# Optimization experiments

Hardware: AMD Instinct MI355X
Metric: run time of the kernel (lower is better)

## Reference

```python
import jax, jax.numpy as jnp
import numpy as np

VOXEL_SIZE = 0.05  # init kwarg


def setup_inputs() -> dict:
    key = jax.random.key(0)
    N, B = 4_194_304, 16
    # coords uniform in [0, 5)^3 -> ~100^3 voxel cells per scene at voxel_size=0.05
    coord = jax.random.uniform(key, (N, 3), dtype=jnp.float32) * 5.0
    # cumulative batch offsets (equal-sized scenes), as pointops expects
    offset = (jnp.arange(1, B + 1, dtype=jnp.int32) * (N // B)).astype(jnp.int32)
    return {"coord": coord, "offset": offset}


def _voxel_mean(coord, offset, voxel_size):
    """Faithful jax port of voxelize_helper + segment_csr(mean) + batch2offset.

    Returns:
      n_p    [N,3]  voxel-mean coords, padded with zeros beyond n_voxels
      n_o    [B]    cumulative voxel counts per batch (batch2offset)
      counts [N]    points per voxel (idx_ptr = concat([0], cumsum(counts[valid])))
    """
    N = coord.shape[0]
    B = offset.shape[0]
    # batch id per point from cumulative offsets
    batch = jnp.searchsorted(offset, jnp.arange(N), side='right')  # [N]
    # start = per-batch min coord (start=None path of voxelize_helper)
    start = jax.ops.segment_min(coord, batch, num_segments=B)      # [B,3]
    grid = jnp.floor((coord - start[batch]) / voxel_size).astype(jnp.int32)  # [N,3]
    G = jnp.max(grid) + 1  # grid extent (per-axis upper bound)
    # linearized cluster key: unique per (batch, gx, gy, gz)
    ckey = ((batch * G + grid[:, 0]) * G + grid[:, 1]) * G + grid[:, 2]
    fill = B * G * G * G  # sentinel beyond any real key
    # sorted unique cluster keys == CSR segment order after sorting cluster indices
    uniq, inv = jnp.unique(ckey, return_inverse=True, size=N, fill_value=fill)
    # fused gather + segment-mean (equivalent to coord[sorted_idx] -> segment_csr mean)
    seg_sum = jax.ops.segment_sum(coord, inv, num_segments=N)                 # [N,3]
    counts = jax.ops.segment_sum(jnp.ones((N,), coord.dtype), inv, num_segments=N)
    n_p = seg_sum / jnp.maximum(counts, 1.0)[:, None]
    # batch id per voxel -> batch2offset (cumulative voxel counts)
    valid = uniq < fill
    vbatch = jnp.where(valid, uniq // (G * G * G), B)
    per_batch = jax.ops.segment_sum(valid.astype(jnp.int32), vbatch, num_segments=B + 1)[:B]
    n_o = jnp.cumsum(per_batch)
    return n_p, n_o, counts.astype(jnp.int32)


def reference(coord, offset):
    return _voxel_mean(coord, offset, VOXEL_SIZE)
```

## Files before the change

kernel.cpp:

```cpp
#include <hip/hip_runtime.h>
#include <stdint.h>


typedef unsigned int uint;
typedef unsigned long long u64;

#define VS 0.05f
#define QSCALE (4096.0f / VS)
#define QINV  (VS / 4096.0f)
#define NBUCKET 2048
#define NBLK_P 256
#define DENSE_MAX 8192

__device__ __forceinline__ uint f2m(float f) {
    uint b = __float_as_uint(f);
    return (b & 0x80000000u) ? ~b : (b | 0x80000000u);
}
__device__ __forceinline__ float m2f(uint m) {
    uint b = (m & 0x80000000u) ? (m & 0x7fffffffu) : ~m;
    return __uint_as_float(b);
}

__global__ void k_init(uint* start_m, int B3) {
    int i = blockIdx.x * blockDim.x + threadIdx.x;
    if (i < B3) start_m[i] = 0xFFFFFFFFu;
}

__global__ void __launch_bounds__(256)
k_minmax(const float* __restrict__ coord, const int* __restrict__ offset,
         int N, int B, uint* start_m) {
    __shared__ uint smin[768];
    __shared__ int soff[256];
    int t = threadIdx.x;
    int nb3 = B * 3;
    for (int j = t; j < B; j += 256) soff[j] = offset[j];
    for (int j = t; j < nb3; j += 256) smin[j] = 0xFFFFFFFFu;
    __syncthreads();

    int F = 3 * N;
    int NQ = F >> 2;
    int per = (NQ + gridDim.x - 1) / gridDim.x;
    int qlo = blockIdx.x * per;
    int qhi = min(NQ, qlo + per);
    const float4* __restrict__ c4 = reinterpret_cast<const float4*>(coord);

    bool fast = false;
    int bU = 0;
    if (qlo < qhi) {
        int pF = (4 * qlo) / 3;
        int pL = (4 * qhi - 1) / 3;
        int bF = 0, bL = 0;
        for (int j = 0; j < B; ++j) {
            bF += (pF >= soff[j]) ? 1 : 0;
            bL += (pL >= soff[j]) ? 1 : 0;
        }
        fast = (bF == bL);
        bU = bF;
    }

    if (fast) {
        int q = qlo + t;
        int p0 = q % 3;
        float s0 = INFINITY, s1 = INFINITY, s2 = INFINITY;
        for (;;) {
            if (q >= qhi) break;
            float4 v = c4[q];
            s0 = fminf(s0, fminf(v.x, v.w)); s1 = fminf(s1, v.y); s2 = fminf(s2, v.z);
            q += 256;
            if (q >= qhi) break;
            v = c4[q];
            s1 = fminf(s1, fminf(v.x, v.w)); s2 = fminf(s2, v.y); s0 = fminf(s0, v.z);
            q += 256;
            if (q >= qhi) break;
            v = c4[q];
            s2 = fminf(s2, fminf(v.x, v.w)); s0 = fminf(s0, v.y); s1 = fminf(s1, v.z);
            q += 256;
        }
        float ax, ay, az;
        if (p0 == 0)      { ax = s0; ay = s1; az = s2; }
        else if (p0 == 1) { ax = s2; ay = s0; az = s1; }
        else              { ax = s1; ay = s2; az = s0; }
        for (int d = 32; d; d >>= 1) {
            ax = fminf(ax, __shfl_xor(ax, d));
            ay = fminf(ay, __shfl_xor(ay, d));
            az = fminf(az, __shfl_xor(az, d));
        }
        if ((t & 63) == 0 && ax < INFINITY) {
            atomicMin(&smin[bU * 3 + 0], f2m(ax));
            atomicMin(&smin[bU * 3 + 1], f2m(ay));
            atomicMin(&smin[bU * 3 + 2], f2m(az));
        }
    } else {
        for (int q = qlo + t; q < qhi; q += 256) {
            float4 v = c4[q];
            int e = 4 * q;
            float vals[4] = {v.x, v.y, v.z, v.w};
#pragma unroll
            for (int k = 0; k < 4; ++k) {
                int ee = e + k;
                int pt = ee / 3;
                int axis = ee - 3 * pt;
                int b = 0;
                for (int j = 0; j < B; ++j) b += (pt >= soff[j]) ? 1 : 0;
                atomicMin(&smin[b * 3 + axis], f2m(vals[k]));
            }
        }
    }

    if (blockIdx.x == 0) {
        for (int ee = 4 * NQ + t; ee < F; ee += 256) {
            int pt = ee / 3;
            int axis = ee - 3 * pt;
            int b = 0;
            for (int j = 0; j < B; ++j) b += (pt >= soff[j]) ? 1 : 0;
            atomicMin(&smin[b * 3 + axis], f2m(coord[ee]));
        }
    }
    __syncthreads();
    for (int j = t; j < nb3; j += 256) {
        uint mn = smin[j];
        if (mn != 0xFFFFFFFFu) atomicMin(&start_m[j], mn);
    }
}


__global__ void __launch_bounds__(1024)
k_count(const float* __restrict__ coord, const int* __restrict__ offset,
        int N, int B, const uint* __restrict__ start_m, uint* __restrict__ histm) {
    __shared__ uint hist[NBUCKET];
    __shared__ int soff[16];
    __shared__ float sstart[48];
    int t = threadIdx.x;
    if (t < B) soff[t] = offset[t];
    if (t < B * 3) sstart[t] = m2f(start_m[t]);
    for (int j = t; j < NBUCKET; j += 1024) hist[j] = 0;
    __syncthreads();
    int chunk = (N + gridDim.x - 1) / gridDim.x;
    int lo = blockIdx.x * chunk, hi = min(N, lo + chunk);
    int bLo = 0, bHi = 0;
    for (int j = 0; j < B; ++j) {
        bLo += (lo >= soff[j]) ? 1 : 0;
        bHi += (hi - 1 >= soff[j]) ? 1 : 0;
    }
    if (lo < hi && bLo == bHi && (lo & 3) == 0) {
        int b = bLo;
        float sx = sstart[b * 3];
        int base = b << 7;
        const float4* __restrict__ c4 = reinterpret_cast<const float4*>(coord);
        int gEnd = hi >> 2;
        for (int g = (lo >> 2) + t; g < gEnd; g += 1024) {
            float4 v0 = c4[3 * g], v1 = c4[3 * g + 1], v2 = c4[3 * g + 2];
            int gx0 = min((int)floorf((v0.x - sx) / VS), 127);
            int gx1 = min((int)floorf((v0.w - sx) / VS), 127);
            int gx2 = min((int)floorf((v1.z - sx) / VS), 127);
            int gx3 = min((int)floorf((v2.y - sx) / VS), 127);
            atomicAdd(&hist[base | gx0], 1u);
            atomicAdd(&hist[base | gx1], 1u);
            atomicAdd(&hist[base | gx2], 1u);
            atomicAdd(&hist[base | gx3], 1u);
        }
        for (int i = (gEnd << 2) + t; i < hi; i += 1024) {
            float x = coord[3 * i];
            int gx = min((int)floorf((x - sx) / VS), 127);
            atomicAdd(&hist[base | gx], 1u);
        }
    } else {
        for (int i = lo + t; i < hi; i += 1024) {
            float x = coord[3 * i];
            int b = 0;
            for (int j = 0; j < B; ++j) b += (i >= soff[j]) ? 1 : 0;
            int gx = min((int)floorf((x - sstart[b * 3]) / VS), 127);
            atomicAdd(&hist[(b << 7) | gx], 1u);
        }
    }
    __syncthreads();
    for (int j = t; j < NBUCKET; j += 1024)
        histm[(size_t)j * NBLK_P + blockIdx.x] = hist[j];
}

__global__ void k_scanrow(uint* __restrict__ histm, uint* __restrict__ tot) {
    __shared__ uint sc[256];
    uint* row = histm + (size_t)blockIdx.x * NBLK_P;
    int t = threadIdx.x;
    uint v = row[t];
    sc[t] = v;
    __syncthreads();
    for (int d = 1; d < 256; d <<= 1) {
        uint add = (t >= d) ? sc[t - d] : 0;
        __syncthreads();
        sc[t] += add;
        __syncthreads();
    }
    row[t] = sc[t] - v;
    if (t == 255) tot[blockIdx.x] = sc[255];
}

__global__ void k_scan2048(const uint* __restrict__ in, uint* __restrict__ out) {
    __shared__ uint p[1024];
    int t = threadIdx.x;
    uint a = in[2 * t], bb = in[2 * t + 1];
    p[t] = a + bb;
    __syncthreads();
    for (int d = 1; d < 1024; d <<= 1) {
        uint add = (t >= d) ? p[t - d] : 0;
        __syncthreads();
        p[t] += add;
        __syncthreads();
    }
    uint ex = p[t] - (a + bb);
    out[2 * t] = ex;
    out[2 * t + 1] = ex + a;
    if (t == 1023) out[2048] = p[1023];
}

__global__ void k_scan2048b(const uint* __restrict__ in, uint* __restrict__ out,
                            int B, float* __restrict__ no_out) {
    __shared__ uint p[1024];
    int t = threadIdx.x;
    uint a = in[2 * t], bb = in[2 * t + 1];
    p[t] = a + bb;
    __syncthreads();
    for (int d = 1; d < 1024; d <<= 1) {
        uint add = (t >= d) ? p[t - d] : 0;
        __syncthreads();
        p[t] += add;
        __syncthreads();
    }
    uint ex = p[t] - (a + bb);
    out[2 * t] = ex;
    out[2 * t + 1] = ex + a;
    if (t == 1023) out[2048] = p[1023];
    if (t < B) no_out[t] = (float)p[((t + 1) << 6) - 1];
}

__device__ __forceinline__ void part_point(float x, float y, float z, int b,
                                           float sx, float sy, float sz,
                                           uint* cursor, u64* __restrict__ recs) {
    int gx = min((int)floorf((x - sx) / VS), 127);
    int gy = min((int)floorf((y - sy) / VS), 127);
    int gz = min((int)floorf((z - sz) / VS), 127);
    float fx = fmaxf(x - (sx + (float)gx * VS), 0.0f);
    float fy = fmaxf(y - (sy + (float)gy * VS), 0.0f);
    float fz = fmaxf(z - (sz + (float)gz * VS), 0.0f);
    uint ux = min((uint)(fx * QSCALE + 0.5f), 4095u);
    uint uy = min((uint)(fy * QSCALE + 0.5f), 4095u);
    uint uz = min((uint)(fz * QSCALE + 0.5f), 4095u);
    uint cell = ((uint)gy << 7) | (uint)gz;
    u64 rec = ((u64)cell << 36) | ((u64)ux << 24) | ((u64)uy << 12) | (u64)uz;
    uint q = ((uint)b << 7) | (uint)gx;
    uint slot = atomicAdd(&cursor[q], 1u);
    recs[slot] = rec;
}

__global__ void __launch_bounds__(1024)
k_partition(const float* __restrict__ coord, const int* __restrict__ offset,
            int N, int B, const uint* __restrict__ start_m,
            const uint* __restrict__ histm, const uint* __restrict__ bucket_base,
            u64* __restrict__ recs) {
    __shared__ uint cursor[NBUCKET];
    __shared__ int soff[16];
    __shared__ float sstart[48];
    int t = threadIdx.x;
    if (t < B) soff[t] = offset[t];
    if (t < B * 3) sstart[t] = m2f(start_m[t]);
    for (int j = t; j < NBUCKET; j += 1024)
        cursor[j] = bucket_base[j] + histm[(size_t)j * NBLK_P + blockIdx.x];
    __syncthreads();
    int chunk = (N + gridDim.x - 1) / gridDim.x;
    int lo = blockIdx.x * chunk, hi = min(N, lo + chunk);
    int bLo = 0, bHi = 0;
    for (int j = 0; j < B; ++j) {
        bLo += (lo >= soff[j]) ? 1 : 0;
        bHi += (hi - 1 >= soff[j]) ? 1 : 0;
    }
    if (lo < hi && bLo == bHi && (lo & 3) == 0) {
        int b = bLo;
        float sx = sstart[b * 3 + 0], sy = sstart[b * 3 + 1], sz = sstart[b * 3 + 2];
        const float4* __restrict__ c4 = reinterpret_cast<const float4*>(coord);
        int gEnd = hi >> 2;
        for (int g = (lo >> 2) + t; g < gEnd; g += 1024) {
            float4 v0 = c4[3 * g], v1 = c4[3 * g + 1], v2 = c4[3 * g + 2];
            part_point(v0.x, v0.y, v0.z, b, sx, sy, sz, cursor, recs);
            part_point(v0.w, v1.x, v1.y, b, sx, sy, sz, cursor, recs);
            part_point(v1.z, v1.w, v2.x, b, sx, sy, sz, cursor, recs);
            part_point(v2.y, v2.z, v2.w, b, sx, sy, sz, cursor, recs);
        }
        for (int i = (gEnd << 2) + t; i < hi; i += 1024) {
            float x = coord[3 * i + 0], y = coord[3 * i + 1], z = coord[3 * i + 2];
            part_point(x, y, z, b, sx, sy, sz, cursor, recs);
        }
    } else {
        for (int i = lo + t; i < hi; i += 1024) {
            float x = coord[3 * i + 0], y = coord[3 * i + 1], z = coord[3 * i + 2];
            int b = 0;
            for (int j = 0; j < B; ++j) b += (i >= soff[j]) ? 1 : 0;
            part_point(x, y, z, b, sstart[b * 3 + 0], sstart[b * 3 + 1],
                       sstart[b * 3 + 2], cursor, recs);
        }
    }
}

__global__ void k_vox(const u64* __restrict__ recs, const uint* __restrict__ bucket_base,
                      uint* __restrict__ voxcount, uint* __restrict__ gmask) {
    __shared__ uint bits[512];
    __shared__ uint wsum[4];
    int q = blockIdx.x;
    uint lo = bucket_base[q], hi = bucket_base[q + 1];
    for (int j = threadIdx.x; j < 512; j += blockDim.x) bits[j] = 0;
    __syncthreads();
    for (uint i = lo + threadIdx.x; i < hi; i += blockDim.x) {
        uint c = (uint)(recs[i] >> 36);
        atomicOr(&bits[c >> 5], 1u << (c & 31));
    }
    __syncthreads();
    uint s = 0;
    for (int w = threadIdx.x; w < 512; w += blockDim.x) {
        uint m = bits[w];
        gmask[(size_t)q * 512 + w] = m;
        s += __popc(m);
    }
    for (int d = 32; d; d >>= 1) s += __shfl_xor(s, d);
    if ((threadIdx.x & 63) == 0) wsum[threadIdx.x >> 6] = s;
    __syncthreads();
    if (threadIdx.x == 0) voxcount[q] = wsum[0] + wsum[1] + wsum[2] + wsum[3];
}

__global__ void __launch_bounds__(1024)
k_emit2(const u64* __restrict__ recs, const uint* __restrict__ bucket_base,
        const uint* __restrict__ voxscan, const uint* __restrict__ gmask,
        const uint* __restrict__ start_m, int N, int B, int out_total,
        float* __restrict__ np_out, float* __restrict__ cnt_out,
        float* __restrict__ out) {
    int t = threadIdx.x;
    if (blockIdx.x >= NBUCKET) {
        uint total = voxscan[NBUCKET];
        int zb = blockIdx.x - NBUCKET;
        int stride = (gridDim.x - NBUCKET) * 1024;
        int tid = zb * 1024 + t;
        for (int j = 3 * (int)total + tid; j < 3 * N; j += stride) np_out[j] = 0.0f;
        for (int j = (int)total + tid; j < N; j += stride) cnt_out[j] = 0.0f;
        for (int j = 4 * N + B + tid; j < out_total; j += stride) out[j] = 0.0f;
        return;
    }
    __shared__ u64 dense[DENSE_MAX];
    __shared__ uint mask[512], wrank[512];
    __shared__ uint wtot[8], woff[9];
    __shared__ float sstart[48];
    int q = blockIdx.x;
    uint lo = bucket_base[q], hi = bucket_base[q + 1];
    if (lo == hi) return;
    if (t < 48) sstart[t] = m2f(start_m[t]);
    uint m = 0, c = 0;
    if (t < 512) {
        m = gmask[(size_t)q * 512 + t];
        mask[t] = m;
        c = __popc(m);
    }
    uint sc = c;
    for (int d = 1; d < 64; d <<= 1) {
        uint nb = __shfl_up(sc, d, 64);
        if ((t & 63) >= d) sc += nb;
    }
    if (t < 512 && (t & 63) == 63) wtot[t >> 6] = sc;
    __syncthreads();
    if (t == 0) {
        uint r = 0;
        for (int k = 0; k < 8; ++k) { woff[k] = r; r += wtot[k]; }
        woff[8] = r;
    }
    __syncthreads();
    if (t < 512) wrank[t] = sc - c + woff[t >> 6];
    uint vc = woff[8];
    uint base_r = voxscan[q];
    int b = q >> 7, gx = q & 127;
    float cx = sstart[b * 3 + 0] + (float)gx * VS;
    float sy = sstart[b * 3 + 1], sz = sstart[b * 3 + 2];
    for (uint segbase = 0; segbase < vc; segbase += DENSE_MAX) {
        uint seglen = min(vc - segbase, (uint)DENSE_MAX);
        for (uint j = t; j < seglen; j += 1024) dense[j] = 0ull;
        __syncthreads();
        for (uint i = lo + t; i < hi; i += 1024) {
            u64 rec = recs[i];
            uint cc = (uint)(rec >> 36);
            uint w = cc >> 5, bit = cc & 31;
            uint r = wrank[w] + __popc(mask[w] & ((1u << bit) - 1u));
            if (r >= segbase && r < segbase + seglen) {
                u64 enc = (((rec >> 24) & 0xFFFull) << 46) | (((rec >> 12) & 0xFFFull) << 28)
                        | ((rec & 0xFFFull) << 10) | 1ull;
                atomicAdd(&dense[r - segbase], enc);
            }
        }
        __syncthreads();
        for (uint rr = segbase + t; rr < segbase + seglen; rr += 1024) {
            uint l2 = 0, h2 = 511;
            while (l2 < h2) {
                uint mid = (l2 + h2 + 1) >> 1;
                if (wrank[mid] <= rr) l2 = mid; else h2 = mid - 1;
            }
            uint w = l2;
            uint idx = rr - wrank[w];
            uint mm = mask[w], bit = 0, cp;
            cp = __popc(mm & 0xFFFFu); if (idx >= cp) { idx -= cp; bit += 16; mm >>= 16; }
            cp = __popc(mm & 0xFFu);   if (idx >= cp) { idx -= cp; bit += 8;  mm >>= 8; }
            cp = __popc(mm & 0xFu);    if (idx >= cp) { idx -= cp; bit += 4;  mm >>= 4; }
            cp = __popc(mm & 0x3u);    if (idx >= cp) { idx -= cp; bit += 2;  mm >>= 2; }
            cp = __popc(mm & 0x1u);    if (idx >= cp) { bit += 1; }
            uint cell = (w << 5) + bit;
            uint gy = cell >> 7, gz = cell & 127u;
            u64 p = dense[rr - segbase];
            float cnt = (float)(uint)(p & 1023ull);
            float inv = 1.0f / fmaxf(cnt, 1.0f);
            uint uz = (uint)((p >> 10) & 0x3FFFFull);
            uint uy = (uint)((p >> 28) & 0x3FFFFull);
            uint ux = (uint)(p >> 46);
            uint r_out = base_r + rr;
            np_out[3 * r_out + 0] = cx + ((float)ux * QINV) * inv;
            np_out[3 * r_out + 1] = sy + (float)gy * VS + ((float)uy * QINV) * inv;
            np_out[3 * r_out + 2] = sz + (float)gz * VS + ((float)uz * QINV) * inv;
            cnt_out[r_out] = cnt;
        }
        __syncthreads();
    }
}


__device__ __forceinline__ void point_grid(const float* __restrict__ coord, int i,
                                           const int* soff, const float* sstart, int B,
                                           float& x, float& y, float& z,
                                           int& b, int& gx, int& gy, int& gz) {
    x = coord[3 * i + 0]; y = coord[3 * i + 1]; z = coord[3 * i + 2];
    b = 0;
    for (int j = 0; j < B; ++j) b += (i >= soff[j]) ? 1 : 0;
    gx = min((int)floorf((x - sstart[b * 3 + 0]) / VS), 127);
    gy = min((int)floorf((y - sstart[b * 3 + 1]) / VS), 127);
    gz = min((int)floorf((z - sstart[b * 3 + 2]) / VS), 127);
}

__device__ __forceinline__ u64 frac12(float x, float y, float z,
                                      const float* sstart, int b,
                                      int gx, int gy, int gz) {
    float fx = fmaxf(x - (sstart[b * 3 + 0] + (float)gx * VS), 0.0f);
    float fy = fmaxf(y - (sstart[b * 3 + 1] + (float)gy * VS), 0.0f);
    float fz = fmaxf(z - (sstart[b * 3 + 2] + (float)gz * VS), 0.0f);
    uint ux = min((uint)(fx * QSCALE + 0.5f), 4095u);
    uint uy = min((uint)(fy * QSCALE + 0.5f), 4095u);
    uint uz = min((uint)(fz * QSCALE + 0.5f), 4095u);
    return ((u64)ux << 24) | ((u64)uy << 12) | (u64)uz;
}

__global__ void k_hist(const float* __restrict__ coord, const int* __restrict__ offset,
                       int N, int B, const uint* __restrict__ start_m,
                       uint* __restrict__ mask) {
    __shared__ int soff[256];
    __shared__ float sstart[768];
    for (int j = threadIdx.x; j < B; j += blockDim.x) soff[j] = offset[j];
    for (int j = threadIdx.x; j < B * 3; j += blockDim.x) sstart[j] = m2f(start_m[j]);
    __syncthreads();
    int i = blockIdx.x * blockDim.x + threadIdx.x;
    if (i >= N) return;
    float x, y, z; int b, gx, gy, gz;
    point_grid(coord, i, soff, sstart, B, x, y, z, b, gx, gy, gz);
    uint key = ((uint)b << 21) | ((uint)gx << 14) | ((uint)gy << 7) | (uint)gz;
    atomicOr(&mask[key >> 5], 1u << (key & 31));
}

__global__ void k_scan1(const uint* __restrict__ mask, uint* __restrict__ partial) {
    int base = blockIdx.x * 1024 + threadIdx.x * 4;
    uint4 m = *(const uint4*)(mask + base);
    uint s = __popc(m.x) + __popc(m.y) + __popc(m.z) + __popc(m.w);
    for (int d = 32; d; d >>= 1) s += __shfl_xor(s, d);
    __shared__ uint wsum[4];
    if ((threadIdx.x & 63) == 0) wsum[threadIdx.x >> 6] = s;
    __syncthreads();
    if (threadIdx.x == 0) partial[blockIdx.x] = wsum[0] + wsum[1] + wsum[2] + wsum[3];
}

__global__ void k_scan2(uint* partial, int P, uint* total) {
    __shared__ uint t[256];
    uint carry = 0;
    for (int base = 0; base < P; base += 256) {
        int j = base + threadIdx.x;
        uint v = (j < P) ? partial[j] : 0;
        t[threadIdx.x] = v;
        __syncthreads();
        for (int d = 1; d < 256; d <<= 1) {
            uint add = (threadIdx.x >= d) ? t[threadIdx.x - d] : 0;
            __syncthreads();
            t[threadIdx.x] += add;
            __syncthreads();
        }
        uint inc = t[threadIdx.x];
        uint chunk = t[255];
        if (j < P) partial[j] = carry + inc - v;
        __syncthreads();
        carry += chunk;
    }
    if (threadIdx.x == 0) *total = carry;
}

__global__ void k_scan3(const uint* __restrict__ mask, const uint* __restrict__ partial,
                        uint* __restrict__ wordrank) {
    int base = blockIdx.x * 1024 + threadIdx.x * 4;
    uint4 m = *(const uint4*)(mask + base);
    uint c0 = __popc(m.x), c1 = __popc(m.y), c2 = __popc(m.z), c3 = __popc(m.w);
    uint s = c0 + c1 + c2 + c3;
    __shared__ uint t[256];
    t[threadIdx.x] = s;
    __syncthreads();
    for (int d = 1; d < 256; d <<= 1) {
        uint add = (threadIdx.x >= d) ? t[threadIdx.x - d] : 0;
        __syncthreads();
        t[threadIdx.x] += add;
        __syncthreads();
    }
    uint ex = t[threadIdx.x] - s + partial[blockIdx.x];
    uint4 r;
    r.x = ex; r.y = ex + c0; r.z = ex + c0 + c1; r.w = ex + c0 + c1 + c2;
    *(uint4*)(wordrank + base) = r;
}

__global__ void k_no(const uint* mask, const uint* wordrank, const uint* total,
                     float* no_out, int B, int W) {
    int b = blockIdx.x * blockDim.x + threadIdx.x;
    if (b >= B) return;
    long long idx = (long long)(b + 1) << 21;
    uint w = (uint)(idx >> 5);
    uint v;
    if (w >= (uint)W) v = *total;
    else v = wordrank[w];
    no_out[b] = (float)v;
}

__global__ void k_accum_sparse(const float* __restrict__ coord, const int* __restrict__ offset,
                               int N, int B, const uint* __restrict__ start_m,
                               const uint* __restrict__ mask, const uint* __restrict__ wordrank,
                               u64* __restrict__ packed) {
    __shared__ int soff[256];
    __shared__ float sstart[768];
    for (int j = threadIdx.x; j < B; j += blockDim.x) soff[j] = offset[j];
    for (int j = threadIdx.x; j < B * 3; j += blockDim.x) sstart[j] = m2f(start_m[j]);
    __syncthreads();
    int i = blockIdx.x * blockDim.x + threadIdx.x;
    if (i >= N) return;
    float x, y, z; int b, gx, gy, gz;
    point_grid(coord, i, soff, sstart, B, x, y, z, b, gx, gy, gz);
    uint key = ((uint)b << 21) | ((uint)gx << 14) | ((uint)gy << 7) | (uint)gz;
    uint w = key >> 5, bit = key & 31;
    uint r = wordrank[w] + __popc(mask[w] & ((1u << bit) - 1u));
    u64 f = frac12(x, y, z, sstart, b, gx, gy, gz);
    u64 enc = (((f >> 24) & 0xFFFull) << 46) | (((f >> 12) & 0xFFFull) << 28)
            | ((f & 0xFFFull) << 10) | 1ull;
    atomicAdd(&packed[r], enc);
}

__global__ void k_decode_sparse(const uint* __restrict__ mask, const uint* __restrict__ wordrank,
                                const uint* __restrict__ start_m,
                                const u64* __restrict__ packed, int W,
                                float* __restrict__ np_out, float* __restrict__ cnt_out) {
    __shared__ float sstart[48];
    for (int j = threadIdx.x; j < 48; j += blockDim.x) sstart[j] = m2f(start_m[j]);
    __syncthreads();
    int w = blockIdx.x * blockDim.x + threadIdx.x;
    if (w >= W) return;
    uint m = mask[w];
    if (m == 0) return;
    uint r = wordrank[w];
    uint kbase = (uint)w << 5;
    while (m) {
        uint bit = (uint)__ffs(m) - 1u;
        m &= m - 1u;
        uint key = kbase + bit;
        u64 p = packed[r];
        float cnt = (float)(uint)(p & 1023ull);
        float inv = 1.0f / fmaxf(cnt, 1.0f);
        uint uz = (uint)((p >> 10) & 0x3FFFFull);
        uint uy = (uint)((p >> 28) & 0x3FFFFull);
        uint ux = (uint)(p >> 46);
        uint b = key >> 21;
        uint gx = (key >> 14) & 127u;
        uint gy = (key >> 7) & 127u;
        uint gz = key & 127u;
        np_out[3 * r + 0] = sstart[b * 3 + 0] + (float)gx * VS + ((float)ux * QINV) * inv;
        np_out[3 * r + 1] = sstart[b * 3 + 1] + (float)gy * VS + ((float)uy * QINV) * inv;
        np_out[3 * r + 2] = sstart[b * 3 + 2] + (float)gz * VS + ((float)uz * QINV) * inv;
        cnt_out[r] = cnt;
        ++r;
    }
}

extern "C" void kernel_launch(void* const* d_in, const int* in_sizes, int n_in,
                              void* d_out, int out_size, void* d_ws, size_t ws_size,
                              hipStream_t stream) {
    const float* coord = (const float*)d_in[0];
    const int* offset = (const int*)d_in[1];
    int N = in_sizes[0] / 3;
    int B = in_sizes[1];

    float* out = (float*)d_out;
    float* np_out = out;
    float* no_out = out + (size_t)3 * N;
    float* cnt_out = no_out + B;

    uint8_t* base = (uint8_t*)d_ws;
    uint* start_m = (uint*)base;
    uint* total = start_m + (size_t)B * 3;

    uintptr_t p = (uintptr_t)(total + 1);
    p = (p + 255) & ~(uintptr_t)255;
    uint* histm = (uint*)p;          p += (size_t)NBUCKET * NBLK_P * 4;
    p = (p + 255) & ~(uintptr_t)255;
    uint* tot = (uint*)p;            p += (size_t)NBUCKET * 4;
    p = (p + 255) & ~(uintptr_t)255;
    uint* bucket_base = (uint*)p;    p += (size_t)(NBUCKET + 1) * 4;
    p = (p + 255) & ~(uintptr_t)255;
    uint* voxcount = (uint*)p;       p += (size_t)NBUCKET * 4;
    p = (p + 255) & ~(uintptr_t)255;
    uint* voxscan = (uint*)p;        p += (size_t)(NBUCKET + 1) * 4;
    p = (p + 255) & ~(uintptr_t)255;
    uint* gmask = (uint*)p;          p += (size_t)NBUCKET * 512 * 4;
    p = (p + 255) & ~(uintptr_t)255;
    u64* recs = (u64*)p;             p += (size_t)N * 8;
    size_t need_part = p - (uintptr_t)base;

    k_init<<<(B * 3 + 255) / 256, 256, 0, stream>>>(start_m, B * 3);
    k_minmax<<<2048, 256, 0, stream>>>(coord, offset, N, B, start_m);

    if (B <= 16 && ws_size >= need_part) {
        k_count<<<NBLK_P, 1024, 0, stream>>>(coord, offset, N, B, start_m, histm);
        k_scanrow<<<NBUCKET, 256, 0, stream>>>(histm, tot);
        k_scan2048<<<1, 1024, 0, stream>>>(tot, bucket_base);
        k_partition<<<NBLK_P, 1024, 0, stream>>>(coord, offset, N, B, start_m, histm,
                                                 bucket_base, recs);
        k_vox<<<NBUCKET, 256, 0, stream>>>(recs, bucket_base, voxcount, gmask);
        k_scan2048b<<<1, 1024, 0, stream>>>(voxcount, voxscan, B, no_out);
        k_emit2<<<NBUCKET + 1024, 1024, 0, stream>>>(recs, bucket_base, voxscan, gmask,
                                                     start_m, N, B, out_size,
                                                     np_out, cnt_out, out);
    } else {
        hipMemsetAsync(d_out, 0, (size_t)out_size * sizeof(float), stream);
        size_t W = (size_t)B << 16;
        int nblk1 = (int)(W / 1024);
        uintptr_t sp = (uintptr_t)(total + 1);
        sp = (sp + 255) & ~(uintptr_t)255;
        uint* partial = (uint*)sp;   sp += (size_t)nblk1 * 4;
        sp = (sp + 255) & ~(uintptr_t)255;
        uint* mask = (uint*)sp;      sp += W * 4;
        sp = (sp + 255) & ~(uintptr_t)255;
        uint* wordrank = (uint*)sp;  sp += W * 4;
        sp = (sp + 255) & ~(uintptr_t)255;
        u64* packed = (u64*)sp;
        int nb = (N + 255) / 256;
        hipMemsetAsync(mask, 0, W * sizeof(uint), stream);
        hipMemsetAsync(packed, 0, (size_t)N * sizeof(u64), stream);
        k_hist<<<nb, 256, 0, stream>>>(coord, offset, N, B, start_m, mask);
        k_scan1<<<nblk1, 256, 0, stream>>>(mask, partial);
        k_scan2<<<1, 256, 0, stream>>>(partial, nblk1, total);
        k_scan3<<<nblk1, 256, 0, stream>>>(mask, partial, wordrank);
        k_no<<<(B + 63) / 64, 64, 0, stream>>>(mask, wordrank, total, no_out, B, (int)W);
        k_accum_sparse<<<nb, 256, 0, stream>>>(coord, offset, N, B, start_m, mask,
                                               wordrank, packed);
        k_decode_sparse<<<(int)((W + 255) / 256), 256, 0, stream>>>(mask, wordrank, start_m,
                                                                    packed, (int)W,
                                                                    np_out, cnt_out);
    }
}
```

Measured before the change: 199.3 us.

## Compute packed records once in count pass and scatter them from temp buffer

The count kernel now computes the full packed voxel record per point, including the bucket id in the top bits, and writes it to a temporary array while building the histogram. A new scatter kernel reads these records and places them with shared-memory cursors, so the coordinates are no longer re-read and the cell math is not recomputed in the partition pass. The cost is an extra N*8-byte write and read of the temp buffer plus more workspace; the consumers now mask the cell field because of the added bucket bits.

```diff
diff --git a/kernel.cpp b/kernel.cpp
--- a/kernel.cpp
+++ b/kernel.cpp
@@ -124,118 +124,9 @@
 }
 
 
-__global__ void __launch_bounds__(1024)
-k_count(const float* __restrict__ coord, const int* __restrict__ offset,
-        int N, int B, const uint* __restrict__ start_m, uint* __restrict__ histm) {
-    __shared__ uint hist[NBUCKET];
-    __shared__ int soff[16];
-    __shared__ float sstart[48];
-    int t = threadIdx.x;
-    if (t < B) soff[t] = offset[t];
-    if (t < B * 3) sstart[t] = m2f(start_m[t]);
-    for (int j = t; j < NBUCKET; j += 1024) hist[j] = 0;
-    __syncthreads();
-    int chunk = (N + gridDim.x - 1) / gridDim.x;
-    int lo = blockIdx.x * chunk, hi = min(N, lo + chunk);
-    int bLo = 0, bHi = 0;
-    for (int j = 0; j < B; ++j) {
-        bLo += (lo >= soff[j]) ? 1 : 0;
-        bHi += (hi - 1 >= soff[j]) ? 1 : 0;
-    }
-    if (lo < hi && bLo == bHi && (lo & 3) == 0) {
-        int b = bLo;
-        float sx = sstart[b * 3];
-        int base = b << 7;
-        const float4* __restrict__ c4 = reinterpret_cast<const float4*>(coord);
-        int gEnd = hi >> 2;
-        for (int g = (lo >> 2) + t; g < gEnd; g += 1024) {
-            float4 v0 = c4[3 * g], v1 = c4[3 * g + 1], v2 = c4[3 * g + 2];
-            int gx0 = min((int)floorf((v0.x - sx) / VS), 127);
-            int gx1 = min((int)floorf((v0.w - sx) / VS), 127);
-            int gx2 = min((int)floorf((v1.z - sx) / VS), 127);
-            int gx3 = min((int)floorf((v2.y - sx) / VS), 127);
-            atomicAdd(&hist[base | gx0], 1u);
-            atomicAdd(&hist[base | gx1], 1u);
-            atomicAdd(&hist[base | gx2], 1u);
-            atomicAdd(&hist[base | gx3], 1u);
-        }
-        for (int i = (gEnd << 2) + t; i < hi; i += 1024) {
-            float x = coord[3 * i];
-            int gx = min((int)floorf((x - sx) / VS), 127);
-            atomicAdd(&hist[base | gx], 1u);
-        }
-    } else {
-        for (int i = lo + t; i < hi; i += 1024) {
-            float x = coord[3 * i];
-            int b = 0;
-            for (int j = 0; j < B; ++j) b += (i >= soff[j]) ? 1 : 0;
-            int gx = min((int)floorf((x - sstart[b * 3]) / VS), 127);
-            atomicAdd(&hist[(b << 7) | gx], 1u);
-        }
-    }
-    __syncthreads();
-    for (int j = t; j < NBUCKET; j += 1024)
-        histm[(size_t)j * NBLK_P + blockIdx.x] = hist[j];
-}
-
-__global__ void k_scanrow(uint* __restrict__ histm, uint* __restrict__ tot) {
-    __shared__ uint sc[256];
-    uint* row = histm + (size_t)blockIdx.x * NBLK_P;
-    int t = threadIdx.x;
-    uint v = row[t];
-    sc[t] = v;
-    __syncthreads();
-    for (int d = 1; d < 256; d <<= 1) {
-        uint add = (t >= d) ? sc[t - d] : 0;
-        __syncthreads();
-        sc[t] += add;
-        __syncthreads();
-    }
-    row[t] = sc[t] - v;
-    if (t == 255) tot[blockIdx.x] = sc[255];
-}
-
-__global__ void k_scan2048(const uint* __restrict__ in, uint* __restrict__ out) {
-    __shared__ uint p[1024];
-    int t = threadIdx.x;
-    uint a = in[2 * t], bb = in[2 * t + 1];
-    p[t] = a + bb;
-    __syncthreads();
-    for (int d = 1; d < 1024; d <<= 1) {
-        uint add = (t >= d) ? p[t - d] : 0;
-        __syncthreads();
-        p[t] += add;
-        __syncthreads();
-    }
-    uint ex = p[t] - (a + bb);
-    out[2 * t] = ex;
-    out[2 * t + 1] = ex + a;
-    if (t == 1023) out[2048] = p[1023];
-}
-
-__global__ void k_scan2048b(const uint* __restrict__ in, uint* __restrict__ out,
-                            int B, float* __restrict__ no_out) {
-    __shared__ uint p[1024];
-    int t = threadIdx.x;
-    uint a = in[2 * t], bb = in[2 * t + 1];
-    p[t] = a + bb;
-    __syncthreads();
-    for (int d = 1; d < 1024; d <<= 1) {
-        uint add = (t >= d) ? p[t - d] : 0;
-        __syncthreads();
-        p[t] += add;
-        __syncthreads();
-    }
-    uint ex = p[t] - (a + bb);
-    out[2 * t] = ex;
-    out[2 * t + 1] = ex + a;
-    if (t == 1023) out[2048] = p[1023];
-    if (t < B) no_out[t] = (float)p[((t + 1) << 6) - 1];
-}
-
-__device__ __forceinline__ void part_point(float x, float y, float z, int b,
-                                           float sx, float sy, float sz,
-                                           uint* cursor, u64* __restrict__ recs) {
+__device__ __forceinline__ u64 mk_rec(float x, float y, float z,
+                                      float sx, float sy, float sz,
+                                      int b, uint& q) {
     int gx = min((int)floorf((x - sx) / VS), 127);
     int gy = min((int)floorf((y - sy) / VS), 127);
     int gz = min((int)floorf((z - sz) / VS), 127);
@@ -246,25 +137,30 @@
     uint uy = min((uint)(fy * QSCALE + 0.5f), 4095u);
     uint uz = min((uint)(fz * QSCALE + 0.5f), 4095u);
     uint cell = ((uint)gy << 7) | (uint)gz;
-    u64 rec = ((u64)cell << 36) | ((u64)ux << 24) | ((u64)uy << 12) | (u64)uz;
-    uint q = ((uint)b << 7) | (uint)gx;
-    uint slot = atomicAdd(&cursor[q], 1u);
-    recs[slot] = rec;
+    q = ((uint)b << 7) | (uint)gx;
+    return ((u64)q << 50) | ((u64)cell << 36) | ((u64)ux << 24) | ((u64)uy << 12) | (u64)uz;
+}
+
+__device__ __forceinline__ void count_point(float x, float y, float z, int b,
+                                            float sx, float sy, float sz, int pid,
+                                            uint* hist, u64* __restrict__ tmp) {
+    uint q;
+    u64 rec = mk_rec(x, y, z, sx, sy, sz, b, q);
+    atomicAdd(&hist[q], 1u);
+    tmp[pid] = rec;
 }
 
 __global__ void __launch_bounds__(1024)
-k_partition(const float* __restrict__ coord, const int* __restrict__ offset,
-            int N, int B, const uint* __restrict__ start_m,
-            const uint* __restrict__ histm, const uint* __restrict__ bucket_base,
-            u64* __restrict__ recs) {
-    __shared__ uint cursor[NBUCKET];
+k_count3(const float* __restrict__ coord, const int* __restrict__ offset,
+         int N, int B, const uint* __restrict__ start_m, uint* __restrict__ histm,
+         u64* __restrict__ tmp) {
+    __shared__ uint hist[NBUCKET];
     __shared__ int soff[16];
     __shared__ float sstart[48];
     int t = threadIdx.x;
     if (t < B) soff[t] = offset[t];
     if (t < B * 3) sstart[t] = m2f(start_m[t]);
-    for (int j = t; j < NBUCKET; j += 1024)
-        cursor[j] = bucket_base[j] + histm[(size_t)j * NBLK_P + blockIdx.x];
+    for (int j = t; j < NBUCKET; j += 1024) hist[j] = 0;
     __syncthreads();
     int chunk = (N + gridDim.x - 1) / gridDim.x;
     int lo = blockIdx.x * chunk, hi = min(N, lo + chunk);
@@ -280,23 +176,101 @@
         int gEnd = hi >> 2;
         for (int g = (lo >> 2) + t; g < gEnd; g += 1024) {
             float4 v0 = c4[3 * g], v1 = c4[3 * g + 1], v2 = c4[3 * g + 2];
-            part_point(v0.x, v0.y, v0.z, b, sx, sy, sz, cursor, recs);
-            part_point(v0.w, v1.x, v1.y, b, sx, sy, sz, cursor, recs);
-            part_point(v1.z, v1.w, v2.x, b, sx, sy, sz, cursor, recs);
-            part_point(v2.y, v2.z, v2.w, b, sx, sy, sz, cursor, recs);
+            int p = 4 * g;
+            count_point(v0.x, v0.y, v0.z, b, sx, sy, sz, p + 0, hist, tmp);
+            count_point(v0.w, v1.x, v1.y, b, sx, sy, sz, p + 1, hist, tmp);
+            count_point(v1.z, v1.w, v2.x, b, sx, sy, sz, p + 2, hist, tmp);
+            count_point(v2.y, v2.z, v2.w, b, sx, sy, sz, p + 3, hist, tmp);
         }
         for (int i = (gEnd << 2) + t; i < hi; i += 1024) {
             float x = coord[3 * i + 0], y = coord[3 * i + 1], z = coord[3 * i + 2];
-            part_point(x, y, z, b, sx, sy, sz, cursor, recs);
+            count_point(x, y, z, b, sx, sy, sz, i, hist, tmp);
         }
     } else {
         for (int i = lo + t; i < hi; i += 1024) {
             float x = coord[3 * i + 0], y = coord[3 * i + 1], z = coord[3 * i + 2];
             int b = 0;
             for (int j = 0; j < B; ++j) b += (i >= soff[j]) ? 1 : 0;
-            part_point(x, y, z, b, sstart[b * 3 + 0], sstart[b * 3 + 1],
-                       sstart[b * 3 + 2], cursor, recs);
-        }
+            count_point(x, y, z, b, sstart[b * 3 + 0], sstart[b * 3 + 1],
+                        sstart[b * 3 + 2], i, hist, tmp);
+        }
+    }
+    __syncthreads();
+    for (int j = t; j < NBUCKET; j += 1024)
+        histm[(size_t)j * NBLK_P + blockIdx.x] = hist[j];
+}
+
+__global__ void k_scanrow(uint* __restrict__ histm, uint* __restrict__ tot) {
+    __shared__ uint sc[256];
+    uint* row = histm + (size_t)blockIdx.x * NBLK_P;
+    int t = threadIdx.x;
+    uint v = row[t];
+    sc[t] = v;
+    __syncthreads();
+    for (int d = 1; d < 256; d <<= 1) {
+        uint add = (t >= d) ? sc[t - d] : 0;
+        __syncthreads();
+        sc[t] += add;
+        __syncthreads();
+    }
+    row[t] = sc[t] - v;
+    if (t == 255) tot[blockIdx.x] = sc[255];
+}
+
+__global__ void k_scan2048(const uint* __restrict__ in, uint* __restrict__ out) {
+    __shared__ uint p[1024];
+    int t = threadIdx.x;
+    uint a = in[2 * t], bb = in[2 * t + 1];
+    p[t] = a + bb;
+    __syncthreads();
+    for (int d = 1; d < 1024; d <<= 1) {
+        uint add = (t >= d) ? p[t - d] : 0;
+        __syncthreads();
+        p[t] += add;
+        __syncthreads();
+    }
+    uint ex = p[t] - (a + bb);
+    out[2 * t] = ex;
+    out[2 * t + 1] = ex + a;
+    if (t == 1023) out[2048] = p[1023];
+}
+
+__global__ void k_scan2048b(const uint* __restrict__ in, uint* __restrict__ out,
+                            int B, float* __restrict__ no_out) {
+    __shared__ uint p[1024];
+    int t = threadIdx.x;
+    uint a = in[2 * t], bb = in[2 * t + 1];
+    p[t] = a + bb;
+    __syncthreads();
+    for (int d = 1; d < 1024; d <<= 1) {
+        uint add = (t >= d) ? p[t - d] : 0;
+        __syncthreads();
+        p[t] += add;
+        __syncthreads();
+    }
+    uint ex = p[t] - (a + bb);
+    out[2 * t] = ex;
+    out[2 * t + 1] = ex + a;
+    if (t == 1023) out[2048] = p[1023];
+    if (t < B) no_out[t] = (float)p[((t + 1) << 6) - 1];
+}
+
+__global__ void __launch_bounds__(1024)
+k_scatter(const u64* __restrict__ tmp, int N,
+          const uint* __restrict__ histm, const uint* __restrict__ bucket_base,
+          u64* __restrict__ recs) {
+    __shared__ uint cursor[NBUCKET];
+    int t = threadIdx.x;
+    for (int j = t; j < NBUCKET; j += 1024)
+        cursor[j] = bucket_base[j] + histm[(size_t)j * NBLK_P + blockIdx.x];
+    __syncthreads();
+    int chunk = (N + gridDim.x - 1) / gridDim.x;
+    int lo = blockIdx.x * chunk, hi = min(N, lo + chunk);
+    for (int i = lo + t; i < hi; i += 1024) {
+        u64 r = tmp[i];
+        uint q = (uint)(r >> 50);
+        uint slot = atomicAdd(&cursor[q], 1u);
+        recs[slot] = r;
     }
 }
 
@@ -309,7 +283,7 @@
     for (int j = threadIdx.x; j < 512; j += blockDim.x) bits[j] = 0;
     __syncthreads();
     for (uint i = lo + threadIdx.x; i < hi; i += blockDim.x) {
-        uint c = (uint)(recs[i] >> 36);
+        uint c = (uint)(recs[i] >> 36) & 0x3FFFu;
         atomicOr(&bits[c >> 5], 1u << (c & 31));
     }
     __syncthreads();
@@ -381,7 +355,7 @@
         __syncthreads();
         for (uint i = lo + t; i < hi; i += 1024) {
             u64 rec = recs[i];
-            uint cc = (uint)(rec >> 36);
+            uint cc = (uint)(rec >> 36) & 0x3FFFu;
             uint w = cc >> 5, bit = cc & 31;
             uint r = wrank[w] + __popc(mask[w] & ((1u << bit) - 1u));
             if (r >= segbase && r < segbase + seglen) {
@@ -620,17 +594,18 @@
     uint* gmask = (uint*)p;          p += (size_t)NBUCKET * 512 * 4;
     p = (p + 255) & ~(uintptr_t)255;
     u64* recs = (u64*)p;             p += (size_t)N * 8;
+    p = (p + 255) & ~(uintptr_t)255;
+    u64* tmp = (u64*)p;              p += (size_t)N * 8;
     size_t need_part = p - (uintptr_t)base;
 
     k_init<<<(B * 3 + 255) / 256, 256, 0, stream>>>(start_m, B * 3);
     k_minmax<<<2048, 256, 0, stream>>>(coord, offset, N, B, start_m);
 
     if (B <= 16 && ws_size >= need_part) {
-        k_count<<<NBLK_P, 1024, 0, stream>>>(coord, offset, N, B, start_m, histm);
+        k_count3<<<NBLK_P, 1024, 0, stream>>>(coord, offset, N, B, start_m, histm, tmp);
         k_scanrow<<<NBUCKET, 256, 0, stream>>>(histm, tot);
         k_scan2048<<<1, 1024, 0, stream>>>(tot, bucket_base);
-        k_partition<<<NBLK_P, 1024, 0, stream>>>(coord, offset, N, B, start_m, histm,
-                                                 bucket_base, recs);
+        k_scatter<<<NBLK_P, 1024, 0, stream>>>(tmp, N, histm, bucket_base, recs);
         k_vox<<<NBUCKET, 256, 0, stream>>>(recs, bucket_base, voxcount, gmask);
         k_scan2048b<<<1, 1024, 0, stream>>>(voxcount, voxscan, B, no_out);
         k_emit2<<<NBUCKET + 1024, 1024, 0, stream>>>(recs, bucket_base, voxscan, gmask,
```

Result: no change. 199.1 us (-0.1%).
